# Kernel tuning notes

Measured on AMD Instinct MI355X. Metric: run time of the kernel, lower is better.

The kernel has to match this reference:

```python
import jax, jax.numpy as jnp
import numpy as np

B, FEAT = 2048, 256
NUM_PIDS, CQ_SIZE = 30000, 8192
MOMENTUM = 0.5
SCALAR = 30.0
EPS_BN = 1e-5      # BatchNorm1d default eps
EPS_NORM = 1e-12   # F.normalize default eps


def l2norm(x):
    n = jnp.linalg.norm(x, axis=1, keepdims=True)
    return x / jnp.maximum(n, EPS_NORM)


def setup_inputs() -> dict:
    key = jax.random.key(0)
    k1, k2, k3, k4 = jax.random.split(key, 4)
    inputs = jax.random.normal(k1, (B, FEAT), jnp.float32)
    label = jax.random.randint(k2, (B,), 0, NUM_PIDS + 1)  # NUM_PIDS == ignore_index
    lut = jax.random.normal(k3, (NUM_PIDS, FEAT), jnp.float32)
    cq = jax.random.normal(k4, (CQ_SIZE, FEAT), jnp.float32)
    bn_weight = jnp.ones((FEAT,), jnp.float32)
    bn_bias = jnp.zeros((FEAT,), jnp.float32)
    return {"inputs": inputs, "label": label, "lut": lut, "cq": cq,
            "bn_weight": bn_weight, "bn_bias": bn_bias}


def reference(inputs, label, lut, cq, bn_weight, bn_bias):
    dtype = inputs.dtype
    rows = jnp.arange(B)

    # --- eval-mode BN on inputs (running stats at init: mean=0, var=1) ---
    norm_inputs = inputs / jnp.sqrt(jnp.asarray(1.0 + EPS_BN, dtype)) * bn_weight + bn_bias

    # --- bad-row masks (rows that are all zero) ---
    bad_lut_mask = jnp.all(lut == 0, axis=1)            # [P]
    good_lut = ~bad_lut_mask
    lc = jnp.minimum(label, NUM_PIDS - 1)
    bad_pos_mask = (label < NUM_PIDS) & bad_lut_mask[lc]  # label hits a bad lut row

    # --- train-mode masked BN over good lut rows (momentum=1.0 => running stats = batch stats) ---
    gm = good_lut[:, None].astype(dtype)
    n = jnp.sum(gm)
    mean = jnp.sum(lut * gm, axis=0) / n
    var = jnp.sum(((lut - mean) ** 2) * gm, axis=0) / n  # biased var for normalization
    lut_bn = jnp.where(good_lut[:, None],
                       (lut - mean) / jnp.sqrt(var + EPS_BN) * bn_weight + bn_bias,
                       lut)
    # running stats update happens under the hood (detached); unbiased var
    rm1 = jax.lax.stop_gradient(mean)
    rv1 = jax.lax.stop_gradient(var * n / (n - 1.0))

    qn = l2norm(norm_inputs)                              # [B, F]
    out_lab = qn @ l2norm(lut_bn).T                       # [B, P]
    out_lab = jnp.where(bad_lut_mask[None, :], jnp.asarray(-1.0, dtype), out_lab)
    out_lab = out_lab.at[rows, lc].set(
        jnp.where(bad_pos_mask, jnp.asarray(1.0, dtype), out_lab[rows, lc]))

    # --- eval-mode masked BN on cq using the just-updated running stats ---
    bad_cq_mask = jnp.all(cq == 0, axis=1)                # [Q]
    cq_bn = jnp.where(~bad_cq_mask[:, None],
                      (cq - rm1) / jnp.sqrt(rv1 + EPS_BN) * bn_weight + bn_bias,
                      cq)
    out_unl = qn @ l2norm(cq_bn).T                        # [B, Q]
    out_unl = jnp.where(bad_cq_mask[None, :], jnp.asarray(-1.0, dtype), out_unl)

    projected = jnp.concatenate([out_lab, out_unl], axis=1) * jnp.asarray(SCALAR, dtype)

    # --- cross entropy with ignore_index = NUM_PIDS, reduction='none', then sum/B ---
    logp = jax.nn.log_softmax(projected, axis=1)
    valid = label != NUM_PIDS
    per = -logp[rows, jnp.where(valid, label, 0)]
    per = jnp.where(valid, per, jnp.asarray(0.0, dtype))
    loss = jnp.sum(per) / B

    # --- serial momentum scatter into lut + circular-buffer enqueue into cq ---
    xs = jax.lax.stop_gradient(inputs)
    lut0 = jax.lax.stop_gradient(lut)
    cq0 = jax.lax.stop_gradient(cq)

    def step(carry, xy):
        lut_c, cq_c, hdr = carry
        x, y = xy
        is_lab = y < NUM_PIDS
        yc = jnp.minimum(y, NUM_PIDS - 1)
        new_row = jnp.where(is_lab, MOMENTUM * lut_c[yc] + (1.0 - MOMENTUM) * x, lut_c[yc])
        lut_c = lut_c.at[yc].set(new_row)
        cq_row = jnp.where(is_lab, cq_c[hdr], x)
        cq_c = cq_c.at[hdr].set(cq_row)
        hdr = jnp.where(is_lab, hdr, (hdr + 1) % CQ_SIZE)
        return (lut_c, cq_c, hdr), None

    (new_lut, new_cq, _), _ = jax.lax.scan(
        step, (lut0, cq0, jnp.asarray(0, label.dtype)), (xs, label))

    return loss, new_lut, new_cq
```

## Files before the change

### kernel.cpp

```cpp
#include <hip/hip_runtime.h>
#include <math.h>

#define NUM_PIDS 30000
#define CQ_SIZE  8192
#define BATCH    2048
#define FEAT     256
#define EPS_BN   1e-5f
#define EPS_NORM 1e-12f
#define SCALARV  30.0f

#define LUT_PAD  30080
#define NCOL     38272
#define BC       128
#define LUT_TILES 235
#define CT       299
#define RT       16
#define NWG      (CT*RT)
#define NB1      120
#define QPLANE   (BATCH*FEAT)

#define WS_Q1    0
#define WS_CB1   (WS_Q1 + BATCH*FEAT)
#define WS_CB2   (WS_CB1 + BATCH)
#define WS_RN2   (WS_CB2 + BATCH)
#define WS_FLAGS (WS_RN2 + 2*NCOL)
#define WS_PSUM  (WS_FLAGS + LUT_PAD)
#define WS_PSQ   (WS_PSUM + NB1*FEAT)
#define WS_PCNT  (WS_PSQ + NB1*FEAT)
#define WS_A1    (WS_PCNT + 128)
#define WS_B1    (WS_A1 + FEAT)
#define WS_A2    (WS_B1 + FEAT)
#define WS_B2    (WS_A2 + FEAT)
#define WS_ZT    (WS_B2 + FEAT)
#define WS_PART  (WS_ZT + BATCH)
#define WS_LOSS8 (WS_PART + BATCH*CT)
#define WS_XH    ((WS_LOSS8 + 8 + 3) & ~3)
#define WS_XL    (WS_XH + NCOL*FEAT/2)
#define WS_QP    (WS_XL + NCOL*FEAT/2)

typedef __bf16 bf16x8 __attribute__((ext_vector_type(8)));
typedef float  f32x4  __attribute__((ext_vector_type(4)));

__device__ __forceinline__ unsigned short f2bf(float f) {
  __bf16 h = (__bf16)f; return __builtin_bit_cast(unsigned short, h);
}
__device__ __forceinline__ float bf2f(unsigned short u) {
  __bf16 h = __builtin_bit_cast(__bf16, u); return (float)h;
}
__device__ __forceinline__ void gload_lds16(const void* g, void* l) {
  __builtin_amdgcn_global_load_lds((__attribute__((address_space(1))) void*)(g),
                                   (__attribute__((address_space(3))) void*)(l), 16, 0, 0);
}

__global__ __launch_bounds__(256) void k_stats1(const float* __restrict__ lut,
                                                float* __restrict__ ws,
                                                int* __restrict__ flags) {
  const int t = threadIdx.x;
  const int rbase = blockIdx.x * 250;
  __shared__ unsigned char wz[250 * 4];
  float s = 0.f, sq = 0.f;
  for (int i = 0; i < 250; ++i) {
    float v = lut[(size_t)(rbase + i) * FEAT + t];
    s += v; sq += v * v;
    unsigned long long bal = __ballot(v != 0.0f);
    if ((t & 63) == 0) wz[i * 4 + (t >> 6)] = (bal != 0ull) ? 1 : 0;
  }
  __syncthreads();
  for (int i = t; i < 250; i += 256) {
    int bad = !(wz[i*4] | wz[i*4+1] | wz[i*4+2] | wz[i*4+3]);
    flags[rbase + i] = bad;
  }
  ws[WS_PSUM + blockIdx.x * FEAT + t] = s;
  ws[WS_PSQ  + blockIdx.x * FEAT + t] = sq;
  if (t == 0) {
    int cnt = 0;
    for (int i = 0; i < 250; ++i)
      cnt += (wz[i*4] | wz[i*4+1] | wz[i*4+2] | wz[i*4+3]) ? 1 : 0;
    ws[WS_PCNT + blockIdx.x] = (float)cnt;
  }
}

__global__ __launch_bounds__(256) void k_stats2(const float* __restrict__ bnw,
                                                const float* __restrict__ bnb,
                                                float* __restrict__ ws) {
  const int t = threadIdx.x;
  float2* rn2 = (float2*)(ws + WS_RN2);
  float s = 0.f, sq = 0.f, n = 0.f;
  for (int b = 0; b < NB1; ++b) { s += ws[WS_PSUM + b*FEAT + t]; sq += ws[WS_PSQ + b*FEAT + t]; }
  for (int b = 0; b < NB1; ++b) n += ws[WS_PCNT + b];
  float mean = s / n;
  float var = fmaxf(sq / n - mean * mean, 0.f);
  float istd_b = rsqrtf(var + EPS_BN);
  float rv1 = var * n / (n - 1.f);
  float istd_u = rsqrtf(rv1 + EPS_BN);
  float w = bnw[t], b_ = bnb[t];
  float a1 = istd_b * w, a2 = istd_u * w;
  ws[WS_A1 + t] = a1; ws[WS_B1 + t] = b_ - mean * a1;
  ws[WS_A2 + t] = a2; ws[WS_B2 + t] = b_ - mean * a2;
  if (t < (LUT_PAD - NUM_PIDS)) rn2[NUM_PIDS + t] = make_float2(0.f, -1e30f);
}

__global__ __launch_bounds__(256) void k_split(const float* __restrict__ lut,
                                               const float* __restrict__ cq,
                                               unsigned short* __restrict__ xh,
                                               unsigned short* __restrict__ xl) {
  const int stride = gridDim.x * blockDim.x;
  for (int u = blockIdx.x * blockDim.x + threadIdx.x; u < NCOL * 32; u += stride) {
    int col = u >> 5, k8 = (u & 31) * 8;
    float v[8];
    if (col < NUM_PIDS) {
      const float4* p = (const float4*)&lut[(size_t)col * FEAT + k8];
      float4 a = p[0], b = p[1];
      v[0]=a.x; v[1]=a.y; v[2]=a.z; v[3]=a.w; v[4]=b.x; v[5]=b.y; v[6]=b.z; v[7]=b.w;
    } else if (col < LUT_PAD) {
#pragma unroll
      for (int j = 0; j < 8; ++j) v[j] = 0.f;
    } else {
      const float4* p = (const float4*)&cq[(size_t)(col - LUT_PAD) * FEAT + k8];
      float4 a = p[0], b = p[1];
      v[0]=a.x; v[1]=a.y; v[2]=a.z; v[3]=a.w; v[4]=b.x; v[5]=b.y; v[6]=b.z; v[7]=b.w;
    }
    unsigned int hp[4], lp[4];
#pragma unroll
    for (int j = 0; j < 4; ++j) {
      unsigned short h0 = f2bf(v[2*j]),   h1 = f2bf(v[2*j+1]);
      unsigned short l0 = f2bf(v[2*j]   - bf2f(h0));
      unsigned short l1 = f2bf(v[2*j+1] - bf2f(h1));
      hp[j] = (unsigned int)h0 | ((unsigned int)h1 << 16);
      lp[j] = (unsigned int)l0 | ((unsigned int)l1 << 16);
    }
    size_t off = (size_t)col * FEAT + k8;
    *(uint4*)(xh + off) = make_uint4(hp[0], hp[1], hp[2], hp[3]);
    *(uint4*)(xl + off) = make_uint4(lp[0], lp[1], lp[2], lp[3]);
  }
}

__global__ __launch_bounds__(256) void k_qn(const float* __restrict__ inp,
                                            const float* __restrict__ bnw,
                                            const float* __restrict__ bnb,
                                            float* __restrict__ ws,
                                            unsigned short* __restrict__ qp) {
  const int r = blockIdx.x, t = threadIdx.x;
  const float s0 = rsqrtf(1.0f + EPS_BN);
  float v = inp[(size_t)r * FEAT + t];
  float bn = v * (bnw[t] * s0) + bnb[t];
  float x = bn * bn;
  for (int o = 32; o; o >>= 1) x += __shfl_down(x, o);
  __shared__ float w4[4];
  __shared__ float w8[8];
  if ((t & 63) == 0) w4[t >> 6] = x;
  __syncthreads();
  float nsq = w4[0] + w4[1] + w4[2] + w4[3];
  float rinv = 1.0f / fmaxf(sqrtf(nsq), EPS_NORM);
  float qn = bn * rinv;
  float y1 = qn * ws[WS_B1 + t], y2 = qn * ws[WS_B2 + t];
  for (int o = 32; o; o >>= 1) { y1 += __shfl_down(y1, o); y2 += __shfl_down(y2, o); }
  if ((t & 63) == 0) { w8[t >> 6] = y1; w8[4 + (t >> 6)] = y2; }
  float q1 = qn * ws[WS_A1 + t], q2 = qn * ws[WS_A2 + t];
  ws[WS_Q1 + (size_t)r * FEAT + t] = q1;
  size_t o1 = (size_t)r * FEAT + t;
  unsigned short h1 = f2bf(q1), h2 = f2bf(q2);
  qp[0*QPLANE + o1] = h1;
  qp[1*QPLANE + o1] = f2bf(q1 - bf2f(h1));
  qp[2*QPLANE + o1] = h2;
  qp[3*QPLANE + o1] = f2bf(q2 - bf2f(h2));
  __syncthreads();
  if (t == 0) {
    ws[WS_CB1 + r] = w8[0] + w8[1] + w8[2] + w8[3];
    ws[WS_CB2 + r] = w8[4] + w8[5] + w8[6] + w8[7];
  }
}

__global__ __launch_bounds__(256) void k_norms(const float* __restrict__ lut,
                                               const float* __restrict__ cq,
                                               float* __restrict__ ws) {
  const int t = threadIdx.x;
  const int row = blockIdx.x;
  float2* rn2 = (float2*)(ws + WS_RN2);
  const int* flags = (const int*)(ws + WS_FLAGS);
  float a, b, v; int cidx, bad;
  __shared__ unsigned char wzs[4];
  __shared__ float w4[4];
  if (row < NUM_PIDS) {
    v = lut[(size_t)row * FEAT + t];
    a = ws[WS_A1 + t]; b = ws[WS_B1 + t];
    cidx = row;
    bad = flags[row];
  } else {
    int q = row - NUM_PIDS;
    v = cq[(size_t)q * FEAT + t];
    a = ws[WS_A2 + t]; b = ws[WS_B2 + t];
    cidx = LUT_PAD + q;
    unsigned long long bal = __ballot(v != 0.0f);
    if ((t & 63) == 0) wzs[t >> 6] = (bal != 0ull) ? 1 : 0;
    __syncthreads();
    bad = !(wzs[0] | wzs[1] | wzs[2] | wzs[3]);
  }
  float bn = bad ? 0.f : (v * a + b);
  float x = bn * bn;
  for (int o = 32; o; o >>= 1) x += __shfl_down(x, o);
  if ((t & 63) == 0) w4[t >> 6] = x;
  __syncthreads();
  if (t == 0) {
    float nrm = sqrtf(w4[0] + w4[1] + w4[2] + w4[3]);
    rn2[cidx] = bad ? make_float2(0.f, -SCALARV)
                    : make_float2(1.0f / fmaxf(nrm, EPS_NORM), 1e30f);
  }
}

__global__ __launch_bounds__(256) void k_gemm(const unsigned short* __restrict__ xh,
                                              const unsigned short* __restrict__ xl,
                                              const unsigned short* __restrict__ qp,
                                              float* __restrict__ ws) {
  __shared__ __align__(16) unsigned char smem[65536];
  const int tid = threadIdx.x;
  const int w = tid >> 6, l = tid & 63;
  const int bid = blockIdx.x;
  const int sid = (bid & 7) * (NWG / 8) + (bid >> 3);
  const int colT = sid >> 4, rowT = sid & 15;
  const bool islut = colT < LUT_TILES;
  const int colbase = colT * BC;
  const int rowbase = rowT * 128;

  const unsigned short* qh = qp + (islut ? 0 : 2) * QPLANE;
  const unsigned short* ql = qh + QPLANE;

  const int segc = l >> 3, slot = l & 7;
  const int kc8l = slot ^ segc;
  const unsigned short* gsrc;
  unsigned char* lbase;
  int gbase;
  if (w == 0)      { gsrc = xh; lbase = smem;         gbase = colbase; }
  else if (w == 1) { gsrc = xl; lbase = smem + 16384; gbase = colbase; }
  else if (w == 2) { gsrc = qh; lbase = smem + 32768; gbase = rowbase; }
  else             { gsrc = ql; lbase = smem + 49152; gbase = rowbase; }

  const int lc = l & 15, lk = l >> 4;
  const int wr = w >> 1, wc = w & 1;

  f32x4 acc[4][4];
#pragma unroll
  for (int rf = 0; rf < 4; ++rf)
#pragma unroll
    for (int cf = 0; cf < 4; ++cf) { f32x4 z = {0.f,0.f,0.f,0.f}; acc[rf][cf] = z; }

  for (int kc = 0; kc < 4; ++kc) {
    const int kb = kc * 64;
#pragma unroll
    for (int i = 0; i < 16; ++i) {
      const unsigned short* g = gsrc + (size_t)(gbase + i * 8 + segc) * FEAT + kb + kc8l * 8;
      gload_lds16(g, lbase + i * 1024);
    }
    __syncthreads();
#pragma unroll
    for (int ks = 0; ks < 2; ++ks) {
      const int kc8 = ks * 4 + lk;
      const int sA = (kc8 ^ (lc & 7)) * 16;
      bf16x8 ah[4], al[4], bh[4], bl[4];
#pragma unroll
      for (int rf = 0; rf < 4; ++rf) {
        int off = (wr * 64 + rf * 16 + lc) * 128 + sA;
        ah[rf] = *(const bf16x8*)(smem + 32768 + off);
        al[rf] = *(const bf16x8*)(smem + 49152 + off);
      }
#pragma unroll
      for (int cf = 0; cf < 4; ++cf) {
        int off = (wc * 64 + cf * 16 + lc) * 128 + sA;
        bh[cf] = *(const bf16x8*)(smem + off);
        bl[cf] = *(const bf16x8*)(smem + 16384 + off);
      }
#pragma unroll
      for (int rf = 0; rf < 4; ++rf)
#pragma unroll
        for (int cf = 0; cf < 4; ++cf) {
          acc[rf][cf] = __builtin_amdgcn_mfma_f32_16x16x32_bf16(ah[rf], bh[cf], acc[rf][cf], 0, 0, 0);
          acc[rf][cf] = __builtin_amdgcn_mfma_f32_16x16x32_bf16(ah[rf], bl[cf], acc[rf][cf], 0, 0, 0);
          acc[rf][cf] = __builtin_amdgcn_mfma_f32_16x16x32_bf16(al[rf], bh[cf], acc[rf][cf], 0, 0, 0);
        }
    }
    __syncthreads();
  }

  const float* cb = ws + (islut ? WS_CB1 : WS_CB2);
  const float2* rn2 = (const float2*)(ws + WS_RN2);
  float* red = (float*)smem;
#pragma unroll
  for (int rf = 0; rf < 4; ++rf) {
    float cbv[4];
#pragma unroll
    for (int r4 = 0; r4 < 4; ++r4)
      cbv[r4] = cb[rowbase + wr * 64 + rf * 16 + lk * 4 + r4];
    float part[4] = {0.f, 0.f, 0.f, 0.f};
#pragma unroll
    for (int cf = 0; cf < 4; ++cf) {
      float2 rc = rn2[colbase + wc * 64 + cf * 16 + lc];
#pragma unroll
      for (int r4 = 0; r4 < 4; ++r4) {
        float z = SCALARV * rc.x * (acc[rf][cf][r4] + cbv[r4]);
        z = fminf(z, rc.y);
        part[r4] += __expf(z - SCALARV);
      }
    }
#pragma unroll
    for (int r4 = 0; r4 < 4; ++r4) {
#pragma unroll
      for (int o = 1; o < 16; o <<= 1) part[r4] += __shfl_xor(part[r4], o);
      if (lc == 0) red[(wr * 64 + rf * 16 + lk * 4 + r4) * 2 + wc] = part[r4];
    }
  }
  __syncthreads();
  if (tid < 128) {
    float val = red[tid * 2] + red[tid * 2 + 1];
    ws[WS_PART + (size_t)(rowbase + tid) * CT + colT] = val;
  }
}

__global__ __launch_bounds__(256) void k_target(const int* __restrict__ label,
                                                const float* __restrict__ lut,
                                                float* __restrict__ ws) {
  const int r = blockIdx.x, t = threadIdx.x;
  const int* flags = (const int*)(ws + WS_FLAGS);
  const float2* rn2 = (const float2*)(ws + WS_RN2);
  int y = label[r];
  if (y >= NUM_PIDS) { if (t == 0) ws[WS_ZT + r] = 0.f; return; }
  if (flags[y] == 1) { if (t == 0) ws[WS_ZT + r] = SCALARV; return; }
  float x = ws[WS_Q1 + (size_t)r * FEAT + t] * lut[(size_t)y * FEAT + t];
  for (int o = 32; o; o >>= 1) x += __shfl_down(x, o);
  __shared__ float w4[4];
  if ((t & 63) == 0) w4[t >> 6] = x;
  __syncthreads();
  if (t == 0) {
    float dot = w4[0] + w4[1] + w4[2] + w4[3];
    ws[WS_ZT + r] = SCALARV * rn2[y].x * (dot + ws[WS_CB1 + r]);
  }
}

__global__ __launch_bounds__(256) void k_loss(const int* __restrict__ label,
                                              float* __restrict__ ws) {
  const int t = threadIdx.x;
  const int r = blockIdx.x * 256 + t;
  const int* flags = (const int*)(ws + WS_FLAGS);
  float ls = 0.f;
  int y = label[r];
  if (y < NUM_PIDS) {
    float ss = 0.f;
    const float* p = ws + WS_PART + (size_t)r * CT;
    for (int c = 0; c < CT; ++c) ss += p[c];
    if (flags[y] == 1) ss += 1.0f - __expf(-2.0f * SCALARV);
    ls = (SCALARV + __logf(ss)) - ws[WS_ZT + r];
  }
  for (int o = 32; o; o >>= 1) ls += __shfl_down(ls, o);
  __shared__ float w4[4];
  if ((t & 63) == 0) w4[t >> 6] = ls;
  __syncthreads();
  if (t == 0) ws[WS_LOSS8 + blockIdx.x] = w4[0] + w4[1] + w4[2] + w4[3];
}

__global__ void k_loss2(float* __restrict__ ws, float* __restrict__ out) {
  if (threadIdx.x == 0) {
    float s = 0.f;
    for (int i = 0; i < 8; ++i) s += ws[WS_LOSS8 + i];
    out[0] = s / (float)BATCH;
  }
}

__global__ __launch_bounds__(256) void k_lutupd(const int* __restrict__ label,
                                                const float* __restrict__ inp,
                                                const float* __restrict__ lut,
                                                float* __restrict__ out_lut) {
  const int r = blockIdx.x, t = threadIdx.x;
  const int y = label[r];
  if (y >= NUM_PIDS) return;
  __shared__ unsigned long long mask[32];
  const int wv = t >> 6, ln = t & 63;
#pragma unroll
  for (int it = 0; it < 8; ++it) {
    int i = it * 256 + wv * 64 + ln;
    unsigned long long bal = __ballot(label[i] == y);
    if (ln == 0) mask[it * 4 + wv] = bal;
  }
  __syncthreads();
  const int wr_ = r >> 6, br_ = r & 63;
  unsigned long long selfbit = 1ull << br_;
  bool after = (mask[wr_] & ~((selfbit - 1) | selfbit)) != 0ull;
  for (int w2 = wr_ + 1; w2 < 32; ++w2) after = after || (mask[w2] != 0ull);
  if (after) return;
  float f = lut[(size_t)y * FEAT + t];
  for (int w2 = 0; w2 <= wr_; ++w2) {
    unsigned long long m = mask[w2];
    if (w2 == wr_) m &= (selfbit - 1) | selfbit;
    while (m) {
      int b = __ffsll((unsigned long long)m) - 1;
      m &= m - 1;
      int rr = w2 * 64 + b;
      f = 0.5f * f + 0.5f * inp[(size_t)rr * FEAT + t];
    }
  }
  out_lut[(size_t)y * FEAT + t] = f;
}

__global__ __launch_bounds__(256) void k_cqupd(const int* __restrict__ label,
                                               const float* __restrict__ inp,
                                               float* __restrict__ out_cq) {
  const int r = blockIdx.x, t = threadIdx.x;
  if (label[r] != NUM_PIDS) return;
  __shared__ unsigned long long mask[32];
  const int wv = t >> 6, ln = t & 63;
#pragma unroll
  for (int it = 0; it < 8; ++it) {
    int i = it * 256 + wv * 64 + ln;
    unsigned long long bal = __ballot(label[i] == NUM_PIDS);
    if (ln == 0) mask[it * 4 + wv] = bal;
  }
  __syncthreads();
  const int wr_ = r >> 6, br_ = r & 63;
  int rank = 0;
  for (int w2 = 0; w2 < wr_; ++w2) rank += __popcll(mask[w2]);
  rank += __popcll(mask[wr_] & ((1ull << br_) - 1ull));
  out_cq[(size_t)rank * FEAT + t] = inp[(size_t)r * FEAT + t];
}

extern "C" void kernel_launch(void* const* d_in, const int* in_sizes, int n_in,
                              void* d_out, int out_size, void* d_ws, size_t ws_size,
                              hipStream_t stream) {
  const float* inp = (const float*)d_in[0];
  const int* label = (const int*)d_in[1];
  const float* lut = (const float*)d_in[2];
  const float* cq  = (const float*)d_in[3];
  const float* bnw = (const float*)d_in[4];
  const float* bnb = (const float*)d_in[5];
  float* out = (float*)d_out;
  float* ws  = (float*)d_ws;
  int* flags = (int*)(ws + WS_FLAGS);
  unsigned short* xh = (unsigned short*)(ws + WS_XH);
  unsigned short* xl = (unsigned short*)(ws + WS_XL);
  unsigned short* qp = (unsigned short*)(ws + WS_QP);

  float* out_lut = out + 1;
  float* out_cq  = out + 1 + (size_t)NUM_PIDS * FEAT;

  hipMemcpyAsync(out_lut, lut, (size_t)NUM_PIDS * FEAT * sizeof(float),
                 hipMemcpyDeviceToDevice, stream);
  hipMemcpyAsync(out_cq, cq, (size_t)CQ_SIZE * FEAT * sizeof(float),
                 hipMemcpyDeviceToDevice, stream);

  k_split<<<2048, 256, 0, stream>>>(lut, cq, xh, xl);
  k_stats1<<<NB1, 256, 0, stream>>>(lut, ws, flags);
  k_stats2<<<1, 256, 0, stream>>>(bnw, bnb, ws);
  k_qn<<<BATCH, 256, 0, stream>>>(inp, bnw, bnb, ws, qp);
  k_norms<<<NUM_PIDS + CQ_SIZE, 256, 0, stream>>>(lut, cq, ws);
  k_gemm<<<NWG, 256, 0, stream>>>(xh, xl, qp, ws);
  k_target<<<BATCH, 256, 0, stream>>>(label, lut, ws);
  k_loss<<<8, 256, 0, stream>>>(label, ws);
  k_loss2<<<1, 64, 0, stream>>>(ws, out);
  k_lutupd<<<BATCH, 256, 0, stream>>>(label, inp, lut, out_lut);
  k_cqupd<<<BATCH, 256, 0, stream>>>(label, inp, out_cq);
}
```

Before: 390.8 us.

## Double-buffer GEMM LDS staging, warp-per-row norms, transpose partials, more stats blocks

```diff
diff --git a/kernel.cpp b/kernel.cpp
--- a/kernel.cpp
+++ b/kernel.cpp
@@ -16,7 +16,8 @@
 #define CT       299
 #define RT       16
 #define NWG      (CT*RT)
-#define NB1      120
+#define NB1      240
+#define ROWS1    125
 #define QPLANE   (BATCH*FEAT)
 
 #define WS_Q1    0
@@ -27,7 +28,7 @@
 #define WS_PSUM  (WS_FLAGS + LUT_PAD)
 #define WS_PSQ   (WS_PSUM + NB1*FEAT)
 #define WS_PCNT  (WS_PSQ + NB1*FEAT)
-#define WS_A1    (WS_PCNT + 128)
+#define WS_A1    (WS_PCNT + 256)
 #define WS_B1    (WS_A1 + FEAT)
 #define WS_A2    (WS_B1 + FEAT)
 #define WS_B2    (WS_A2 + FEAT)
@@ -51,22 +52,27 @@
   __builtin_amdgcn_global_load_lds((__attribute__((address_space(1))) void*)(g),
                                    (__attribute__((address_space(3))) void*)(l), 16, 0, 0);
 }
+__device__ __forceinline__ void stage8(const unsigned short* g, unsigned char* d) {
+#pragma unroll
+  for (int i = 0; i < 8; ++i)
+    gload_lds16(g + (size_t)i * 16 * FEAT, d + i * 1024);
+}
 
 __global__ __launch_bounds__(256) void k_stats1(const float* __restrict__ lut,
                                                 float* __restrict__ ws,
                                                 int* __restrict__ flags) {
   const int t = threadIdx.x;
-  const int rbase = blockIdx.x * 250;
-  __shared__ unsigned char wz[250 * 4];
+  const int rbase = blockIdx.x * ROWS1;
+  __shared__ unsigned char wz[ROWS1 * 4];
   float s = 0.f, sq = 0.f;
-  for (int i = 0; i < 250; ++i) {
+  for (int i = 0; i < ROWS1; ++i) {
     float v = lut[(size_t)(rbase + i) * FEAT + t];
     s += v; sq += v * v;
     unsigned long long bal = __ballot(v != 0.0f);
     if ((t & 63) == 0) wz[i * 4 + (t >> 6)] = (bal != 0ull) ? 1 : 0;
   }
   __syncthreads();
-  for (int i = t; i < 250; i += 256) {
+  for (int i = t; i < ROWS1; i += 256) {
     int bad = !(wz[i*4] | wz[i*4+1] | wz[i*4+2] | wz[i*4+3]);
     flags[rbase + i] = bad;
   }
@@ -74,7 +80,7 @@
   ws[WS_PSQ  + blockIdx.x * FEAT + t] = sq;
   if (t == 0) {
     int cnt = 0;
-    for (int i = 0; i < 250; ++i)
+    for (int i = 0; i < ROWS1; ++i)
       cnt += (wz[i*4] | wz[i*4+1] | wz[i*4+2] | wz[i*4+3]) ? 1 : 0;
     ws[WS_PCNT + blockIdx.x] = (float)cnt;
   }
@@ -174,37 +180,28 @@
 __global__ __launch_bounds__(256) void k_norms(const float* __restrict__ lut,
                                                const float* __restrict__ cq,
                                                float* __restrict__ ws) {
-  const int t = threadIdx.x;
-  const int row = blockIdx.x;
+  const int row = blockIdx.x * 4 + (threadIdx.x >> 6);
+  const int ln = threadIdx.x & 63;
+  if (row >= NUM_PIDS + CQ_SIZE) return;
   float2* rn2 = (float2*)(ws + WS_RN2);
-  const int* flags = (const int*)(ws + WS_FLAGS);
-  float a, b, v; int cidx, bad;
-  __shared__ unsigned char wzs[4];
-  __shared__ float w4[4];
+  const float* src; const float* av; const float* bv; int cidx;
   if (row < NUM_PIDS) {
-    v = lut[(size_t)row * FEAT + t];
-    a = ws[WS_A1 + t]; b = ws[WS_B1 + t];
-    cidx = row;
-    bad = flags[row];
+    src = lut + (size_t)row * FEAT; av = ws + WS_A1; bv = ws + WS_B1; cidx = row;
   } else {
     int q = row - NUM_PIDS;
-    v = cq[(size_t)q * FEAT + t];
-    a = ws[WS_A2 + t]; b = ws[WS_B2 + t];
-    cidx = LUT_PAD + q;
-    unsigned long long bal = __ballot(v != 0.0f);
-    if ((t & 63) == 0) wzs[t >> 6] = (bal != 0ull) ? 1 : 0;
-    __syncthreads();
-    bad = !(wzs[0] | wzs[1] | wzs[2] | wzs[3]);
-  }
-  float bn = bad ? 0.f : (v * a + b);
-  float x = bn * bn;
-  for (int o = 32; o; o >>= 1) x += __shfl_down(x, o);
-  if ((t & 63) == 0) w4[t >> 6] = x;
-  __syncthreads();
-  if (t == 0) {
-    float nrm = sqrtf(w4[0] + w4[1] + w4[2] + w4[3]);
-    rn2[cidx] = bad ? make_float2(0.f, -SCALARV)
-                    : make_float2(1.0f / fmaxf(nrm, EPS_NORM), 1e30f);
+    src = cq + (size_t)q * FEAT; av = ws + WS_A2; bv = ws + WS_B2; cidx = LUT_PAD + q;
+  }
+  float4 x = ((const float4*)src)[ln];
+  float4 a = ((const float4*)av)[ln];
+  float4 b = ((const float4*)bv)[ln];
+  bool nz = (x.x != 0.f) || (x.y != 0.f) || (x.z != 0.f) || (x.w != 0.f);
+  unsigned long long bal = __ballot(nz);
+  float t0 = a.x*x.x + b.x, t1 = a.y*x.y + b.y, t2 = a.z*x.z + b.z, t3 = a.w*x.w + b.w;
+  float ssum = t0*t0 + t1*t1 + t2*t2 + t3*t3;
+  for (int o = 32; o; o >>= 1) ssum += __shfl_xor(ssum, o);
+  if (ln == 0) {
+    rn2[cidx] = (bal == 0ull) ? make_float2(0.f, -SCALARV)
+                              : make_float2(1.0f / fmaxf(sqrtf(ssum), EPS_NORM), 1e30f);
   }
 }
 
@@ -225,8 +222,6 @@
   const unsigned short* qh = qp + (islut ? 0 : 2) * QPLANE;
   const unsigned short* ql = qh + QPLANE;
 
-  const int segc = l >> 3, slot = l & 7;
-  const int kc8l = slot ^ segc;
   const unsigned short* gsrc;
   unsigned char* lbase;
   int gbase;
@@ -235,8 +230,12 @@
   else if (w == 2) { gsrc = qh; lbase = smem + 32768; gbase = rowbase; }
   else             { gsrc = ql; lbase = smem + 49152; gbase = rowbase; }
 
+  const int kchunk = (l & 3) ^ ((l >> 4) & 3);
+  const unsigned short* gp = gsrc + (size_t)(gbase + (l >> 2)) * FEAT + kchunk * 8;
+
   const int lc = l & 15, lk = l >> 4;
   const int wr = w >> 1, wc = w & 1;
+  const int roff = (lk ^ ((lc >> 2) & 3)) * 16;
 
   f32x4 acc[4][4];
 #pragma unroll
@@ -244,41 +243,39 @@
 #pragma unroll
     for (int cf = 0; cf < 4; ++cf) { f32x4 z = {0.f,0.f,0.f,0.f}; acc[rf][cf] = z; }
 
-  for (int kc = 0; kc < 4; ++kc) {
-    const int kb = kc * 64;
-#pragma unroll
-    for (int i = 0; i < 16; ++i) {
-      const unsigned short* g = gsrc + (size_t)(gbase + i * 8 + segc) * FEAT + kb + kc8l * 8;
-      gload_lds16(g, lbase + i * 1024);
-    }
-    __syncthreads();
-#pragma unroll
-    for (int ks = 0; ks < 2; ++ks) {
-      const int kc8 = ks * 4 + lk;
-      const int sA = (kc8 ^ (lc & 7)) * 16;
-      bf16x8 ah[4], al[4], bh[4], bl[4];
-#pragma unroll
-      for (int rf = 0; rf < 4; ++rf) {
-        int off = (wr * 64 + rf * 16 + lc) * 128 + sA;
-        ah[rf] = *(const bf16x8*)(smem + 32768 + off);
-        al[rf] = *(const bf16x8*)(smem + 49152 + off);
+  stage8(gp, lbase);
+  for (int s = 0; s < 8; ++s) {
+    const int cur = s & 1;
+    if (s < 7) {
+      stage8(gp + (s + 1) * 32, lbase + (cur ^ 1) * 8192);
+      asm volatile("s_waitcnt vmcnt(8)" ::: "memory");
+    } else {
+      asm volatile("s_waitcnt vmcnt(0)" ::: "memory");
+    }
+    __builtin_amdgcn_s_barrier();
+    __builtin_amdgcn_sched_barrier(0);
+    bf16x8 ah[4], al[4], bh[4], bl[4];
+#pragma unroll
+    for (int rf = 0; rf < 4; ++rf) {
+      int off = cur * 8192 + (wr * 64 + rf * 16 + lc) * 64 + roff;
+      ah[rf] = *(const bf16x8*)(smem + 32768 + off);
+      al[rf] = *(const bf16x8*)(smem + 49152 + off);
+    }
+#pragma unroll
+    for (int cf = 0; cf < 4; ++cf) {
+      int off = cur * 8192 + (wc * 64 + cf * 16 + lc) * 64 + roff;
+      bh[cf] = *(const bf16x8*)(smem + off);
+      bl[cf] = *(const bf16x8*)(smem + 16384 + off);
+    }
+#pragma unroll
+    for (int rf = 0; rf < 4; ++rf)
+#pragma unroll
+      for (int cf = 0; cf < 4; ++cf) {
+        acc[rf][cf] = __builtin_amdgcn_mfma_f32_16x16x32_bf16(ah[rf], bh[cf], acc[rf][cf], 0, 0, 0);
+        acc[rf][cf] = __builtin_amdgcn_mfma_f32_16x16x32_bf16(ah[rf], bl[cf], acc[rf][cf], 0, 0, 0);
+        acc[rf][cf] = __builtin_amdgcn_mfma_f32_16x16x32_bf16(al[rf], bh[cf], acc[rf][cf], 0, 0, 0);
       }
-#pragma unroll
-      for (int cf = 0; cf < 4; ++cf) {
-        int off = (wc * 64 + cf * 16 + lc) * 128 + sA;
-        bh[cf] = *(const bf16x8*)(smem + off);
-        bl[cf] = *(const bf16x8*)(smem + 16384 + off);
-      }
-#pragma unroll
-      for (int rf = 0; rf < 4; ++rf)
-#pragma unroll
-        for (int cf = 0; cf < 4; ++cf) {
-          acc[rf][cf] = __builtin_amdgcn_mfma_f32_16x16x32_bf16(ah[rf], bh[cf], acc[rf][cf], 0, 0, 0);
-          acc[rf][cf] = __builtin_amdgcn_mfma_f32_16x16x32_bf16(ah[rf], bl[cf], acc[rf][cf], 0, 0, 0);
-          acc[rf][cf] = __builtin_amdgcn_mfma_f32_16x16x32_bf16(al[rf], bh[cf], acc[rf][cf], 0, 0, 0);
-        }
-    }
-    __syncthreads();
+    if (s < 7) __builtin_amdgcn_s_barrier();
   }
 
   const float* cb = ws + (islut ? WS_CB1 : WS_CB2);
@@ -311,7 +308,7 @@
   __syncthreads();
   if (tid < 128) {
     float val = red[tid * 2] + red[tid * 2 + 1];
-    ws[WS_PART + (size_t)(rowbase + tid) * CT + colT] = val;
+    ws[WS_PART + (size_t)colT * BATCH + rowbase + tid] = val;
   }
 }
 
@@ -344,8 +341,8 @@
   int y = label[r];
   if (y < NUM_PIDS) {
     float ss = 0.f;
-    const float* p = ws + WS_PART + (size_t)r * CT;
-    for (int c = 0; c < CT; ++c) ss += p[c];
+    const float* p = ws + WS_PART;
+    for (int c = 0; c < CT; ++c) ss += p[(size_t)c * BATCH + r];
     if (flags[y] == 1) ss += 1.0f - __expf(-2.0f * SCALARV);
     ls = (SCALARV + __logf(ss)) - ws[WS_ZT + r];
   }
@@ -448,7 +445,7 @@
   k_stats1<<<NB1, 256, 0, stream>>>(lut, ws, flags);
   k_stats2<<<1, 256, 0, stream>>>(bnw, bnb, ws);
   k_qn<<<BATCH, 256, 0, stream>>>(inp, bnw, bnb, ws, qp);
-  k_norms<<<NUM_PIDS + CQ_SIZE, 256, 0, stream>>>(lut, cq, ws);
+  k_norms<<<(NUM_PIDS + CQ_SIZE + 3) / 4, 256, 0, stream>>>(lut, cq, ws);
   k_gemm<<<NWG, 256, 0, stream>>>(xh, xl, qp, ws);
   k_target<<<BATCH, 256, 0, stream>>>(label, lut, ws);
   k_loss<<<8, 256, 0, stream>>>(label, ws);
```

Result: faster. 374.0 us (-4.3%).
